# Performance work log

Measured on AMD Instinct MI355X. Metric: run time of the kernel, lower is better.

The kernel has to match this reference:

```python
import jax, jax.numpy as jnp
import numpy as np
from jax.scipy.special import logsumexp

B, T, D = 256, 2048, 64


def setup_inputs() -> dict:
    key = jax.random.key(0)
    k1, k2, k3, k4 = jax.random.split(key, 4)
    p = jax.random.normal(k1, (B, T, D), dtype=jnp.float32)
    labels = jax.random.randint(k2, (B, T), 0, D)
    y = jax.nn.one_hot(labels, D, dtype=jnp.int32)  # [B,T,D] one-hot labels
    # valid lengths in [T//2, T]; mask == 1 marks padding positions
    lengths = jax.random.randint(k3, (B,), T // 2, T + 1)
    mask = (jnp.arange(T)[None, :] >= lengths[:, None]).astype(jnp.int32)
    transition = 0.1 * jax.random.normal(k4, (D, D), dtype=jnp.float32)
    return {"p": p, "y": y, "mask": mask, "transition": transition}


def reference(p, y, mask, transition):
    # CRF negative log-likelihood per example: logZ - emission_score - transition_score
    Bb = p.shape[0]
    valid = (1 - mask).astype(jnp.float32)            # [B,T], 1 = valid token
    y1 = y.astype(jnp.float32) * valid[:, :, None]    # masked one-hot labels
    s1 = jnp.sum(y1 * p, axis=(1, 2))                 # emission score
    pair = jnp.einsum('btd,bte->bde', y1[:, :-1], y1[:, 1:])  # label bigram counts
    s2 = jnp.sum(pair * transition, axis=(1, 2))      # transition score

    # forward algorithm: alpha_t = p_t + logsumexp(alpha_{t-1}[:, :, None] + T)
    def step(state, inp):
        new = inp + logsumexp(state[:, :, None] + transition[None, :, :], axis=1)
        return new, new

    xs = jnp.moveaxis(p[:, 1:, :], 1, 0)              # [T-1, B, D]
    _, a1 = jax.lax.scan(step, p[:, 0, :], xs)        # a1: [T-1, B, D]

    # index of alpha at the last valid timestep (length L -> a1 index L-2)
    m1 = jnp.argmin(
        jnp.concatenate([valid.astype(jnp.int32), jnp.zeros((Bb, 1), jnp.int32)], axis=1),
        axis=1) - 2                                   # [B]
    last = a1[m1, jnp.arange(Bb)]                     # [B, D]
    logZ = logsumexp(last, axis=-1)
    return logZ - s1 - s2
```

## Files before the change

### kernel.cpp

```cpp
#include <hip/hip_runtime.h>
#include <stdint.h>
#include <string.h>

#define BB 256
#define TT 2048
#define DD 64
#define CC 128
#define SS 16
#define C_L2E 1.44269504f
#define C_LN2 0.69314718f
#define C_BIAS 0.0028174f

typedef short sh8  __attribute__((ext_vector_type(8)));
typedef float f32x4 __attribute__((ext_vector_type(4)));

union BU { sh8 v8; unsigned int u[4]; unsigned short s[8]; };

__device__ __forceinline__ float expf_fast(float x) { return __builtin_amdgcn_exp2f(x * C_L2E); }
__device__ __forceinline__ unsigned short bf16rne(float x) {
    unsigned int u = __float_as_uint(x);
    u += 0x7FFF + ((u >> 16) & 1u);
    return (unsigned short)(u >> 16);
}
__device__ __forceinline__ unsigned int pkbf(float hi, float lo) {
    return __builtin_amdgcn_perm(__float_as_uint(hi), __float_as_uint(lo), 0x07060302u);
}
__device__ __forceinline__ void gl_lds16(void* l, const void* g) {
    __builtin_amdgcn_global_load_lds(
        (const __attribute__((address_space(1))) unsigned int*)g,
        (__attribute__((address_space(3))) unsigned int*)l, 16, 0, 0);
}

#define DPPMAX(x, ctrl, rm, bm) { int _xi = __float_as_int(x);                              \
    int _yi = __builtin_amdgcn_update_dpp(_xi, _xi, ctrl, rm, bm, false);                   \
    x = fmaxf(x, __int_as_float(_yi)); }

__global__ __launch_bounds__(256) void crf_score(
    const float* __restrict__ p, const int* __restrict__ y,
    const int* __restrict__ mask, const float* __restrict__ tr,
    float* __restrict__ wsS, int* __restrict__ wsL)
{
    __shared__ int mk[257];
    __shared__ unsigned char labs[257];
    __shared__ float redf[4];
    __shared__ int redi[4];
    const int c = blockIdx.y, t0 = blockIdx.x * 256;
    const int tid = threadIdx.x;
    const int g = tid & 15, sub = tid >> 4;
    const size_t cb = (size_t)c * TT;

    mk[tid] = mask[cb + t0 + tid];
    if (tid == 0) mk[256] = (t0 + 256 < TT) ? mask[cb + t0 + 256] : 1;
    __syncthreads();

    float s1 = 0.f;
    int vc = 0;
#pragma unroll
    for (int k = 0; k < 16; ++k) {
        const int ti = k * 16 + sub;
        if (mk[ti] == 0) {
            int4 v = ((const int4*)y)[(cb + t0 + ti) * 16 + g];
            int cand = v.w ? 4 * g + 3 : v.z ? 4 * g + 2 : v.y ? 4 * g + 1 : v.x ? 4 * g : -1;
#pragma unroll
            for (int xm = 1; xm <= 8; xm <<= 1) {
                int o = __shfl_xor(cand, xm, 16);
                cand = o > cand ? o : cand;
            }
            if (g == 0) {
                labs[ti] = (unsigned char)cand;
                s1 += p[(cb + t0 + ti) * DD + cand];
                vc += 1;
            }
        }
    }
    if (tid < 16 && mk[256] == 0) {
        int4 v = ((const int4*)y)[(cb + t0 + 256) * 16 + tid];
        int cand = v.w ? 4 * tid + 3 : v.z ? 4 * tid + 2 : v.y ? 4 * tid + 1 : v.x ? 4 * tid : -1;
#pragma unroll
        for (int xm = 1; xm <= 8; xm <<= 1) {
            int o = __shfl_xor(cand, xm, 16);
            cand = o > cand ? o : cand;
        }
        if (tid == 0) labs[256] = (unsigned char)cand;
    }
    __syncthreads();

    float s2 = 0.f;
    if (mk[tid + 1] == 0)
        s2 = tr[(int)labs[tid] * DD + (int)labs[tid + 1]];

    float acc = s1 + s2;
#pragma unroll
    for (int xm = 32; xm >= 1; xm >>= 1) { acc += __shfl_xor(acc, xm, 64); vc += __shfl_xor(vc, xm, 64); }
    if ((tid & 63) == 0) { redf[tid >> 6] = acc; redi[tid >> 6] = vc; }
    __syncthreads();
    if (tid == 0) {
        atomicAdd(&wsS[c], redf[0] + redf[1] + redf[2] + redf[3]);
        atomicAdd(&wsL[c], redi[0] + redi[1] + redi[2] + redi[3]);
    }
}

__global__ __launch_bounds__(128) void crf_probe(
    const float* __restrict__ p, const float* __restrict__ tr,
    const int* __restrict__ wsL,
    unsigned short* __restrict__ wsA, unsigned short* __restrict__ wsB, int* __restrict__ wsSig)
{
    __shared__ char lds[SS * 4096];
    const int tid = threadIdx.x, w = tid >> 6, lane = tid & 63;
    const int q = lane >> 4, ml = lane & 15;
    const int cg = blockIdx.x;
    const int ic = blockIdx.y;
    const int bwd = w;
    const int c = cg * 16 + ml;
    const int Lml = wsL[c];
    const int t0 = ic * SS, t1 = t0 + SS;
    const int ts = (ic == 0) ? 1 : t0;
    const float* prow = p + (size_t)c * TT * DD;

    int mL = Lml;
#pragma unroll
    for (int xm = 32; xm >= 1; xm >>= 1) { int o = __shfl_xor(mL, xm, 64); mL = o > mL ? o : mL; }

    {
        const int mls = lane >> 2, u = lane & 3;
        const int gs = (mls >> 1) & 3;
        const char* gbase = (const char*)(p + (size_t)(cg * 16 + mls) * TT * DD);
        const int lofs = (u ^ gs) << 4;
#pragma unroll
        for (int s = 0; s < 8; ++s) {
            const int tt = w * 8 + s;
            if (t0 + tt < mL) {
                const char* gsrc = gbase + (size_t)(t0 + tt) * 256 + lofs;
                char* ldst = lds + tt * 4096;
#pragma unroll
                for (int k = 0; k < 4; ++k)
                    gl_lds16(ldst + k * 1024, gsrc + k * 64);
            }
        }
    }

    BU A[4][2];
#pragma unroll
    for (int mt = 0; mt < 4; ++mt)
#pragma unroll
        for (int kt2 = 0; kt2 < 2; ++kt2)
#pragma unroll
            for (int j = 0; j < 8; ++j) {
                int lam = 32 * kt2 + 16 * (j >> 2) + 4 * q + (j & 3);
                float tv = bwd ? tr[(16 * mt + ml) * DD + lam] : tr[lam * DD + 16 * mt + ml];
                A[mt][kt2].s[j] = (short)bf16rne(expf_fast(tv));
            }

    float xs[16];
    if (!bwd && ic == 0) {
#pragma unroll
        for (int k = 0; k < 4; ++k) {
            f32x4 v = *(const f32x4*)(prow + 16 * k + 4 * q);
#pragma unroll
            for (int r = 0; r < 4; ++r)
                xs[(k >> 1) * 8 + (k & 1) * 4 + r] = __builtin_amdgcn_exp2f(fmaf(v[r], C_L2E, C_BIAS));
        }
    } else {
#pragma unroll
        for (int i = 0; i < 16; ++i) xs[i] = 1.0f;
    }

    int ibeg = 0, iend = SS;
    if (!bwd) { int ir = mL - t0; if (ir < 0) ir = 0; iend = (ir + 3) & ~3; if (iend > SS) iend = SS; }
    else      { int ir = t1 - mL; if (ir < 0) ir = 0; ibeg = ir & ~3; if (ibeg > SS) ibeg = SS; }

    __syncthreads();

    int sig = 0;
    const f32x4 z4 = {0.f, 0.f, 0.f, 0.f};

    if (ibeg < iend) {
        const char* rbase = lds + ml * 64 + ((q ^ ((ml >> 1) & 3)) << 4);
        for (int ib = ibeg; ib < iend; ib += 4) {
#pragma unroll
            for (int s = 0; s < 4; ++s) {
                const int i = ib + s;
                const int t = bwd ? (t1 - 1 - i) : (t0 + i);
                const int tt = t - t0;
                const bool act = (t >= ts) && (t < Lml);
                f32x4 er[4];
#pragma unroll
                for (int k = 0; k < 4; ++k)
                    er[k] = *(const f32x4*)(rbase + tt * 4096 + k * 1024);
                float ee[4][4];
#pragma unroll
                for (int k = 0; k < 4; ++k)
#pragma unroll
                    for (int r = 0; r < 4; ++r)
                        ee[k][r] = __builtin_amdgcn_exp2f(fmaf(er[k][r], C_L2E, C_BIAS));
                float cand[16];
                BU Bf[2];
                f32x4 acc[4];
                if (!bwd) {
#pragma unroll
                    for (int kt2 = 0; kt2 < 2; ++kt2)
#pragma unroll
                        for (int jj = 0; jj < 4; ++jj)
                            Bf[kt2].u[jj] = pkbf(xs[kt2 * 8 + 2 * jj + 1], xs[kt2 * 8 + 2 * jj]);
#pragma unroll
                    for (int mt = 0; mt < 4; ++mt) {
                        acc[mt] = __builtin_amdgcn_mfma_f32_16x16x32_bf16(A[mt][0].v8, Bf[0].v8, z4, 0, 0, 0);
                        acc[mt] = __builtin_amdgcn_mfma_f32_16x16x32_bf16(A[mt][1].v8, Bf[1].v8, acc[mt], 0, 0, 0);
                    }
#pragma unroll
                    for (int mt = 0; mt < 4; ++mt)
#pragma unroll
                        for (int r = 0; r < 4; ++r)
                            cand[(mt >> 1) * 8 + (mt & 1) * 4 + r] = acc[mt][r] * ee[mt][r];
                } else {
                    float xsc[16];
#pragma unroll
                    for (int kt2 = 0; kt2 < 2; ++kt2)
#pragma unroll
                        for (int h = 0; h < 2; ++h)
#pragma unroll
                            for (int r = 0; r < 4; ++r)
                                xsc[kt2 * 8 + h * 4 + r] = xs[kt2 * 8 + h * 4 + r] * ee[2 * kt2 + h][r];
#pragma unroll
                    for (int kt2 = 0; kt2 < 2; ++kt2)
#pragma unroll
                        for (int jj = 0; jj < 4; ++jj)
                            Bf[kt2].u[jj] = pkbf(xsc[kt2 * 8 + 2 * jj + 1], xsc[kt2 * 8 + 2 * jj]);
#pragma unroll
                    for (int mt = 0; mt < 4; ++mt) {
                        acc[mt] = __builtin_amdgcn_mfma_f32_16x16x32_bf16(A[mt][0].v8, Bf[0].v8, z4, 0, 0, 0);
                        acc[mt] = __builtin_amdgcn_mfma_f32_16x16x32_bf16(A[mt][1].v8, Bf[1].v8, acc[mt], 0, 0, 0);
                    }
#pragma unroll
                    for (int mt = 0; mt < 4; ++mt)
#pragma unroll
                        for (int r = 0; r < 4; ++r)
                            cand[(mt >> 1) * 8 + (mt & 1) * 4 + r] = acc[mt][r];
                }
                if (s == 3) {
                    float mx = fabsf(cand[0]);
#pragma unroll
                    for (int i2 = 1; i2 < 16; ++i2) mx = fmaxf(mx, fabsf(cand[i2]));
                    DPPMAX(mx, 0x111, 0xF, 0xF); DPPMAX(mx, 0x112, 0xF, 0xF);
                    DPPMAX(mx, 0x114, 0xF, 0xF); DPPMAX(mx, 0x118, 0xF, 0xF);
                    DPPMAX(mx, 0x142, 0xA, 0xF); DPPMAX(mx, 0x143, 0xC, 0xF);
                    int smx = __builtin_amdgcn_readlane(__float_as_int(mx), 63);
                    int kk = ((smx >> 23) & 255) - 127;
                    kk = kk < -124 ? -124 : (kk > 124 ? 124 : kk);
                    float sc = __int_as_float((unsigned)(127 - kk) << 23);
#pragma unroll
                    for (int i2 = 0; i2 < 16; ++i2) cand[i2] *= sc;
                    if (act) sig += kk;
                }
#pragma unroll
                for (int i2 = 0; i2 < 16; ++i2) xs[i2] = act ? cand[i2] : xs[i2];
            }
        }
    }

    unsigned short* dst = (bwd ? wsB : wsA) + ((size_t)c * CC + ic) * 64;
#pragma unroll
    for (int kt2 = 0; kt2 < 2; ++kt2)
#pragma unroll
        for (int h = 0; h < 2; ++h)
#pragma unroll
            for (int r = 0; r < 4; ++r)
                dst[32 * kt2 + 16 * h + 4 * q + r] = bf16rne(xs[kt2 * 8 + h * 4 + r]);
    if (!bwd && q == 0) wsSig[c * CC + ic] = sig;
}

__global__ __launch_bounds__(256) void crf_combine(
    const unsigned short* __restrict__ wsA, const unsigned short* __restrict__ wsB,
    const int* __restrict__ wsSig, const float* __restrict__ wsS,
    float* __restrict__ out)
{
    __shared__ float eParts[4];
    const int tid = threadIdx.x, w = tid >> 6, lane = tid & 63;
    const int c = blockIdx.x;

    float Ep = 0.f;
#pragma unroll 4
    for (int k = 0; k < 32; ++k) {
        const int i = w * 32 + k;
        if (i == 0) continue;
        float b  = __uint_as_float((unsigned)wsB[((size_t)c * CC + i) * 64 + lane] << 16);
        float ap = __uint_as_float((unsigned)wsA[((size_t)c * CC + i - 1) * 64 + lane] << 16);
        float d1 = b * ap, d0 = b;
#pragma unroll
        for (int xm = 32; xm >= 1; xm >>= 1) { d1 += __shfl_xor(d1, xm, 64); d0 += __shfl_xor(d0, xm, 64); }
        Ep += (float)wsSig[c * CC + i] + __builtin_amdgcn_logf(d1) - __builtin_amdgcn_logf(d0);
    }
    if (w == 0) Ep += (float)wsSig[c * CC];
    if (w == 3) {
        float al = __uint_as_float((unsigned)wsA[((size_t)c * CC + CC - 1) * 64 + lane] << 16);
#pragma unroll
        for (int xm = 32; xm >= 1; xm >>= 1) al += __shfl_xor(al, xm, 64);
        Ep += __builtin_amdgcn_logf(al);
    }
    if (lane == 0) eParts[w] = Ep;
    __syncthreads();
    if (tid == 0) {
        float E = eParts[0] + eParts[1] + eParts[2] + eParts[3];
        out[c] = C_LN2 * E - wsS[c];
    }
}

extern "C" void kernel_launch(void* const* d_in, const int* in_sizes, int n_in,
                              void* d_out, int out_size, void* d_ws, size_t ws_size,
                              hipStream_t stream) {
    const float* p  = (const float*)d_in[0];
    const int*   y  = (const int*)d_in[1];
    const int*   mk = (const int*)d_in[2];
    const float* tr = (const float*)d_in[3];
    float* out = (float*)d_out;

    float* wsS  = (float*)d_ws;
    int*   wsL  = (int*)((char*)d_ws + 1024);
    int*   wsSg = (int*)((char*)d_ws + 4096);
    unsigned short* wsA = (unsigned short*)((char*)d_ws + (1u << 18));
    unsigned short* wsB = (unsigned short*)((char*)d_ws + (1u << 18) + (4u << 20));

    hipMemsetAsync(d_ws, 0, 2048, stream);
    crf_score<<<dim3(8, BB), dim3(256), 0, stream>>>(p, y, mk, tr, wsS, wsL);
    crf_probe<<<dim3(16, CC), dim3(128), 0, stream>>>(p, tr, wsL, wsA, wsB, wsSg);
    crf_combine<<<dim3(BB), dim3(256), 0, stream>>>(wsA, wsB, wsSg, wsS, out);
}
```

Before: 337.1 us.

## Halve chunk length, pack two chunks per 256-thread block, reswizzle LDS

Chunks shrink from 16 to 8 timesteps, doubling their count to 256, and each 256-thread block now handles two chunks with forward and backward waves each. The global-to-LDS load is rewritten so each row is 256 contiguous bytes with an XOR swizzle on (m&7), and the LDS reads are changed to match. The aim is to shorten the serial per-chunk recurrence and spread the work over more waves. In exchange the combine kernel has twice as many chunk boundaries to merge and the workspace grows.

```diff
diff --git a/kernel.cpp b/kernel.cpp
--- a/kernel.cpp
+++ b/kernel.cpp
@@ -5,8 +5,8 @@
 #define BB 256
 #define TT 2048
 #define DD 64
-#define CC 128
-#define SS 16
+#define CC 256
+#define SS 8
 #define C_L2E 1.44269504f
 #define C_LN2 0.69314718f
 #define C_BIAS 0.0028174f
@@ -100,17 +100,18 @@
     }
 }
 
-__global__ __launch_bounds__(128) void crf_probe(
+__global__ __launch_bounds__(256) void crf_probe(
     const float* __restrict__ p, const float* __restrict__ tr,
     const int* __restrict__ wsL,
     unsigned short* __restrict__ wsA, unsigned short* __restrict__ wsB, int* __restrict__ wsSig)
 {
-    __shared__ char lds[SS * 4096];
+    __shared__ char lds[2 * SS * 4096];
     const int tid = threadIdx.x, w = tid >> 6, lane = tid & 63;
     const int q = lane >> 4, ml = lane & 15;
     const int cg = blockIdx.x;
-    const int ic = blockIdx.y;
-    const int bwd = w;
+    const int pair = w >> 1;
+    const int ic = blockIdx.y * 2 + pair;
+    const int bwd = w & 1;
     const int c = cg * 16 + ml;
     const int Lml = wsL[c];
     const int t0 = ic * SS, t1 = t0 + SS;
@@ -122,19 +123,21 @@
     for (int xm = 32; xm >= 1; xm >>= 1) { int o = __shfl_xor(mL, xm, 64); mL = o > mL ? o : mL; }
 
     {
-        const int mls = lane >> 2, u = lane & 3;
-        const int gs = (mls >> 1) & 3;
-        const char* gbase = (const char*)(p + (size_t)(cg * 16 + mls) * TT * DD);
-        const int lofs = (u ^ gs) << 4;
-#pragma unroll
-        for (int s = 0; s < 8; ++s) {
-            const int tt = w * 8 + s;
+        const int r = lane >> 4, u = lane & 15;
+        char* ldsbase = lds + pair * (SS * 4096);
+#pragma unroll
+        for (int s = 0; s < 4; ++s) {
+            const int tt = bwd * 4 + s;
             if (t0 + tt < mL) {
-                const char* gsrc = gbase + (size_t)(t0 + tt) * 256 + lofs;
-                char* ldst = lds + tt * 4096;
-#pragma unroll
-                for (int k = 0; k < 4; ++k)
-                    gl_lds16(ldst + k * 1024, gsrc + k * 64);
+                char* ldst = ldsbase + tt * 4096;
+#pragma unroll
+                for (int j = 0; j < 4; ++j) {
+                    const int m = 4 * j + r;
+                    const char* gsrc = (const char*)p
+                        + ((size_t)(cg * 16 + m) * TT + (t0 + tt)) * 256
+                        + ((u ^ (m & 7)) << 4);
+                    gl_lds16(ldst + j * 1024, gsrc);
+                }
             }
         }
     }
@@ -175,7 +178,8 @@
     const f32x4 z4 = {0.f, 0.f, 0.f, 0.f};
 
     if (ibeg < iend) {
-        const char* rbase = lds + ml * 64 + ((q ^ ((ml >> 1) & 3)) << 4);
+        const char* rb = lds + pair * (SS * 4096) + ml * 256;
+        const int sx = ml & 7;
         for (int ib = ibeg; ib < iend; ib += 4) {
 #pragma unroll
             for (int s = 0; s < 4; ++s) {
@@ -186,7 +190,7 @@
                 f32x4 er[4];
 #pragma unroll
                 for (int k = 0; k < 4; ++k)
-                    er[k] = *(const f32x4*)(rbase + tt * 4096 + k * 1024);
+                    er[k] = *(const f32x4*)(rb + tt * 4096 + (((4 * k + q) ^ sx) << 4));
                 float ee[4][4];
 #pragma unroll
                 for (int k = 0; k < 4; ++k)
@@ -280,8 +284,8 @@
 
     float Ep = 0.f;
 #pragma unroll 4
-    for (int k = 0; k < 32; ++k) {
-        const int i = w * 32 + k;
+    for (int k = 0; k < CC / 4; ++k) {
+        const int i = w * (CC / 4) + k;
         if (i == 0) continue;
         float b  = __uint_as_float((unsigned)wsB[((size_t)c * CC + i) * 64 + lane] << 16);
         float ap = __uint_as_float((unsigned)wsA[((size_t)c * CC + i - 1) * 64 + lane] << 16);
@@ -317,11 +321,11 @@
     float* wsS  = (float*)d_ws;
     int*   wsL  = (int*)((char*)d_ws + 1024);
     int*   wsSg = (int*)((char*)d_ws + 4096);
-    unsigned short* wsA = (unsigned short*)((char*)d_ws + (1u << 18));
-    unsigned short* wsB = (unsigned short*)((char*)d_ws + (1u << 18) + (4u << 20));
+    unsigned short* wsA = (unsigned short*)((char*)d_ws + (1u << 20));
+    unsigned short* wsB = (unsigned short*)((char*)d_ws + (5u << 20));
 
     hipMemsetAsync(d_ws, 0, 2048, stream);
     crf_score<<<dim3(8, BB), dim3(256), 0, stream>>>(p, y, mk, tr, wsS, wsL);
-    crf_probe<<<dim3(16, CC), dim3(128), 0, stream>>>(p, tr, wsL, wsA, wsB, wsSg);
+    crf_probe<<<dim3(16, CC / 2), dim3(256), 0, stream>>>(p, tr, wsL, wsA, wsB, wsSg);
     crf_combine<<<dim3(BB), dim3(256), 0, stream>>>(wsA, wsB, wsSg, wsS, out);
 }
```

Measured after the change: 342.8 us. Within noise of the previous version (+1.7%).
